# Kernel tuning notes

Measured on AMD Instinct MI355X. Metric: run time of the kernel, lower is better.

The kernel has to match this reference:

```python
import jax, jax.numpy as jnp
import numpy as np

N_NODES = 100000
N_EDGES = 1600000
F_IN, F_HID, F_OUT = 32, 32, 16


def gcn_conv(x, W, b, src, dst):
    """GCNConv: out = D^{-1/2} (A+I) D^{-1/2} X W + b (self-loops already in src/dst)."""
    n = x.shape[0]
    h = x @ W  # [N, F_out]
    deg = jax.ops.segment_sum(jnp.ones(dst.shape[0], x.dtype), dst, num_segments=n)
    dinv = jnp.where(deg > 0, jax.lax.rsqrt(deg), jnp.zeros((), x.dtype))
    coef = dinv[src] * dinv[dst]  # [E_total]
    out = jax.ops.segment_sum(h[src] * coef[:, None], dst, num_segments=n)
    return out + b


def setup_inputs() -> dict:
    key = jax.random.key(0)
    k1, k2, k3, k4, k5, k6, k7 = jax.random.split(key, 7)
    x = jax.random.normal(k1, (N_NODES, F_IN), dtype=jnp.float32)
    edge_index = jax.random.randint(k2, (2, N_EDGES), 0, N_NODES, dtype=jnp.int64)
    s1 = 1.0 / np.sqrt(F_IN)
    s2 = 1.0 / np.sqrt(F_HID)
    W1 = jax.random.uniform(k3, (F_IN, F_HID), jnp.float32, -s1, s1)
    b1 = jax.random.uniform(k4, (F_HID,), jnp.float32, -s1, s1)
    W2 = jax.random.uniform(k5, (F_HID, F_OUT), jnp.float32, -s2, s2)
    b2 = jax.random.uniform(k6, (F_OUT,), jnp.float32, -s2, s2)
    return {"x": x, "edge_index": edge_index, "W1": W1, "b1": b1, "W2": W2, "b2": b2}


def reference(x, edge_index, W1, b1, W2, b2):
    n = x.shape[0]
    loops = jnp.arange(n, dtype=edge_index.dtype)  # GCNConv adds self-loops
    src = jnp.concatenate([edge_index[0], loops])
    dst = jnp.concatenate([edge_index[1], loops])
    h = jnp.tanh(gcn_conv(x, W1, b1, src, dst))
    h = gcn_conv(h, W2, b2, src, dst)
    return h, jax.nn.log_softmax(h, axis=1)
```

## Files before the change

### kernel.cpp

```cpp
#include <hip/hip_runtime.h>
#include <hip/hip_bf16.h>
#include <hip/hip_fp16.h>
#include <math.h>
#include <stdint.h>

#define F_IN  32
#define F_HID 32
#define F_OUT 16
#define NPB     256
#define LOG_NPB 8
#define MAXNB   512
#define BH      256

__device__ inline uint32_t pk_add(uint32_t a, uint32_t b) {
    union { uint32_t u; __half2 h; } x, y, r;
    x.u = a; y.u = b;
    r.h = __hadd2(x.h, y.h);
    return r.u;
}
__device__ inline uint4 pk_add4(uint4 a, uint4 b) {
    a.x = pk_add(a.x, b.x); a.y = pk_add(a.y, b.y);
    a.z = pk_add(a.z, b.z); a.w = pk_add(a.w, b.w);
    return a;
}
__device__ inline uint2 pk_add2(uint2 a, uint2 b) {
    a.x = pk_add(a.x, b.x); a.y = pk_add(a.y, b.y);
    return a;
}

__device__ inline float fexp(float x) {
    return __builtin_amdgcn_exp2f(x * 1.44269504089f);
}
__device__ inline float ftanh(float x) {
    x = fminf(fmaxf(x, -15.f), 15.f);
    float t = __builtin_amdgcn_exp2f(x * 2.88539008178f);
    return (t - 1.0f) * __builtin_amdgcn_rcpf(t + 1.0f);
}

__launch_bounds__(1024)
__global__ void k_hist(const int* __restrict__ ei, int ne, int chunk, int nb,
                       int* __restrict__ hist_mat) {
    __shared__ int hist[MAXNB];
    int t = threadIdx.x, b = blockIdx.x;
    for (int i = t; i < nb; i += 1024) hist[i] = 0;
    __syncthreads();
    long s = (long)b * chunk;
    long e = s + chunk; if (e > ne) e = ne;
    const int* dstp = ei + ne;
    long i = s + (long)t * 4;
    for (; i + 4 <= e; i += 4096) {
        int4 d = *(const int4*)(dstp + i);
        atomicAdd(&hist[d.x >> LOG_NPB], 1);
        atomicAdd(&hist[d.y >> LOG_NPB], 1);
        atomicAdd(&hist[d.z >> LOG_NPB], 1);
        atomicAdd(&hist[d.w >> LOG_NPB], 1);
    }
    if (i < e)
        for (long j = i; j < e; ++j) atomicAdd(&hist[dstp[j] >> LOG_NPB], 1);
    __syncthreads();
    for (int k = t; k < nb; k += 1024)
        hist_mat[(size_t)b * nb + k] = hist[k];
}

__global__ void k_colscan(const int* __restrict__ hist_mat, int* __restrict__ off_mat,
                          int* __restrict__ totalG, int nb) {
    int k = blockIdx.x * 256 + threadIdx.x;
    if (k >= nb) return;
    int run = 0;
    #pragma unroll 8
    for (int b = 0; b < BH; ++b) {
        size_t idx = (size_t)b * nb + k;
        int h = hist_mat[idx];
        off_mat[idx] = run;
        run += h;
    }
    totalG[k] = run;
}

__global__ void k_scanb(const int* __restrict__ totalG, int* __restrict__ boff, int nb) {
    __shared__ int sh[256];
    int t = threadIdx.x;
    int base = t * 2;
    int v[2], s = 0;
    #pragma unroll
    for (int j = 0; j < 2; ++j) {
        v[j] = (base + j < nb) ? totalG[base + j] : 0;
        s += v[j];
    }
    sh[t] = s; __syncthreads();
    for (int o = 1; o < 256; o <<= 1) {
        int u = (t >= o) ? sh[t - o] : 0;
        __syncthreads();
        sh[t] += u;
        __syncthreads();
    }
    int run = sh[t] - s;
    #pragma unroll
    for (int j = 0; j < 2; ++j) {
        int k = base + j;
        if (k < nb) { boff[k] = run; run += v[j]; }
    }
    if (t == 255) boff[nb] = sh[255];
}

__launch_bounds__(1024)
__global__ void k_fillc(const int* __restrict__ ei, int ne, int chunk, int nb,
                        const int* __restrict__ off_mat, const int* __restrict__ boff,
                        uint32_t* __restrict__ ebuf) {
    __shared__ int cur[MAXNB];
    int t = threadIdx.x, b = blockIdx.x;
    for (int i = t; i < nb; i += 1024)
        cur[i] = off_mat[(size_t)b * nb + i] + boff[i];
    __syncthreads();
    long s = (long)b * chunk;
    long e = s + chunk; if (e > ne) e = ne;
    const int* srcp = ei;
    const int* dstp = ei + ne;
    long i = s + (long)t * 4;
    for (; i + 4 <= e; i += 4096) {
        int4 sv = *(const int4*)(srcp + i);
        int4 dv = *(const int4*)(dstp + i);
        int p0 = atomicAdd(&cur[dv.x >> LOG_NPB], 1);
        ebuf[p0] = (uint32_t)sv.x | ((uint32_t)(dv.x & (NPB - 1)) << 17);
        int p1 = atomicAdd(&cur[dv.y >> LOG_NPB], 1);
        ebuf[p1] = (uint32_t)sv.y | ((uint32_t)(dv.y & (NPB - 1)) << 17);
        int p2 = atomicAdd(&cur[dv.z >> LOG_NPB], 1);
        ebuf[p2] = (uint32_t)sv.z | ((uint32_t)(dv.z & (NPB - 1)) << 17);
        int p3 = atomicAdd(&cur[dv.w >> LOG_NPB], 1);
        ebuf[p3] = (uint32_t)sv.w | ((uint32_t)(dv.w & (NPB - 1)) << 17);
    }
    if (i < e) {
        for (long j = i; j < e; ++j) {
            int sn = srcp[j], dn = dstp[j];
            int p = atomicAdd(&cur[dn >> LOG_NPB], 1);
            ebuf[p] = (uint32_t)sn | ((uint32_t)(dn & (NPB - 1)) << 17);
        }
    }
}

__launch_bounds__(256)
__global__ void k_pass2(const uint32_t* __restrict__ ebuf, const int* __restrict__ boff,
                        const float* __restrict__ x,
                        int* __restrict__ csr, int* __restrict__ off_g,
                        float* __restrict__ dinv, uint32_t* __restrict__ xd,
                        int n, int nb) {
    __shared__ int hist[NPB], scn[NPB], cur[NPB];
    __shared__ float sdi[NPB];
    int b = blockIdx.x, t = threadIdx.x;
    int base = boff[b], end = boff[b + 1];
    int v0 = b << LOG_NPB;
    hist[t] = 0;
    __syncthreads();
    for (int i = base + t; i < end; i += 256)
        atomicAdd(&hist[(ebuf[i] >> 17) & (NPB - 1)], 1);
    __syncthreads();
    int val = hist[t];
    scn[t] = val; __syncthreads();
    for (int o = 1; o < 256; o <<= 1) {
        int u = (t >= o) ? scn[t - o] : 0;
        __syncthreads();
        scn[t] += u;
        __syncthreads();
    }
    int excl = scn[t] - val + base;
    cur[t] = excl;
    int v = v0 + t;
    float d = 0.f;
    if (v < n) {
        off_g[v] = excl;
        d = rsqrtf((float)(val + 1));
        dinv[v] = d;
    }
    sdi[t] = d;
    if (b == nb - 1 && t == 0) off_g[n] = end;
    if (b == nb - 1 && t < 16) xd[(size_t)n * 16 + t] = 0u;
    __syncthreads();
    for (int i = base + t; i < end; i += 256) {
        uint32_t r = ebuf[i];
        int slot = atomicAdd(&cur[(r >> 17) & (NPB - 1)], 1);
        csr[slot] = (int)(r & 0x1FFFF);
    }
    for (int i = t; i < NPB * 16; i += 256) {
        int nl = i >> 4, wp = i & 15;
        int vv = v0 + nl;
        if (vv < n) {
            float2 xx = *(const float2*)(x + (size_t)vv * F_IN + 2 * wp);
            float di = sdi[nl];
            union { __half2 h; uint32_t u; } pk;
            pk.h = __floats2half2_rn(xx.x * di, xx.y * di);
            xd[(size_t)vv * 16 + wp] = pk.u;
        }
    }
}

__launch_bounds__(256)
__global__ void k_agg1(const uint32_t* __restrict__ xd, const int* __restrict__ csr,
                       const int* __restrict__ off_g,
                       const float* __restrict__ dinv, const float* __restrict__ b1,
                       const float* __restrict__ W1, const float* __restrict__ W2,
                       uint32_t* __restrict__ g2, int n) {
    __shared__ float W1s[F_IN * F_HID];
    __shared__ float W2s[F_HID * F_OUT];
    __shared__ float sums[8][F_IN + 1];
    __shared__ float hb[8][F_HID + 1];
    int t = threadIdx.x, wv = t >> 6, lane = t & 63;
    ((float4*)W1s)[t] = ((const float4*)W1)[t];
    if (t < 128) ((float4*)W2s)[t] = ((const float4*)W2)[t];
    if (blockIdx.x == 0 && t < 8) g2[(size_t)n * 8 + t] = 0u;
    int half = lane >> 5, l = lane & 31;
    int v = blockIdx.x * 8 + wv * 2 + half;
    bool act = v < n;
    int q = l & 3, slot = l >> 2;
    uint4 acc = make_uint4(0u, 0u, 0u, 0u);
    if (act) {
        if (slot == 0) acc = *(const uint4*)(xd + (size_t)v * 16 + q * 4);
        int start = off_g[v], cnt = off_g[v + 1] - start;
        const int* cp = csr + start;
        int i0 = (slot      < cnt) ? cp[slot]      : n;
        int i1 = (slot + 8  < cnt) ? cp[slot + 8]  : n;
        int i2 = (slot + 16 < cnt) ? cp[slot + 16] : n;
        int i3 = (slot + 24 < cnt) ? cp[slot + 24] : n;
        uint4 w0 = *(const uint4*)(xd + (size_t)i0 * 16 + q * 4);
        uint4 w1 = *(const uint4*)(xd + (size_t)i1 * 16 + q * 4);
        uint4 w2 = *(const uint4*)(xd + (size_t)i2 * 16 + q * 4);
        uint4 w3 = *(const uint4*)(xd + (size_t)i3 * 16 + q * 4);
        acc = pk_add4(acc, w0);
        acc = pk_add4(acc, w1);
        acc = pk_add4(acc, w2);
        acc = pk_add4(acc, w3);
        for (int k = slot + 32; k < cnt; k += 8) {
            int s = cp[k];
            acc = pk_add4(acc, *(const uint4*)(xd + (size_t)s * 16 + q * 4));
        }
    }
    #pragma unroll
    for (int off = 4; off < 32; off <<= 1) {
        acc.x = pk_add(acc.x, (uint32_t)__shfl_xor((int)acc.x, off));
        acc.y = pk_add(acc.y, (uint32_t)__shfl_xor((int)acc.y, off));
        acc.z = pk_add(acc.z, (uint32_t)__shfl_xor((int)acc.z, off));
        acc.w = pk_add(acc.w, (uint32_t)__shfl_xor((int)acc.w, off));
    }
    int ch = l;
    int src = (lane & 32) + (ch >> 3);
    uint32_t a0 = (uint32_t)__shfl((int)acc.x, src);
    uint32_t a1 = (uint32_t)__shfl((int)acc.y, src);
    uint32_t a2 = (uint32_t)__shfl((int)acc.z, src);
    uint32_t a3 = (uint32_t)__shfl((int)acc.w, src);
    int widx = (ch & 7) >> 1;
    uint32_t w = (widx & 2) ? ((widx & 1) ? a3 : a2) : ((widx & 1) ? a1 : a0);
    union { uint32_t u; __half2 h; } pw; pw.u = w;
    float2 f2 = __half22float2(pw.h);
    sums[wv * 2 + half][ch] = (ch & 1) ? f2.y : f2.x;
    __syncthreads();
    {
        int nl = t >> 5, c = t & 31;
        int v1 = blockIdx.x * 8 + nl;
        float di = (v1 < n) ? dinv[v1] : 0.f;
        float s = 0.f;
        #pragma unroll
        for (int k = 0; k < F_IN; ++k) s += sums[nl][k] * W1s[k * F_HID + c];
        hb[nl][c] = ftanh(s * di + b1[c]);
    }
    __syncthreads();
    if (t < 128) {
        int nl = t >> 4, c = t & 15;
        int v2 = blockIdx.x * 8 + nl;
        float s = 0.f;
        #pragma unroll
        for (int k = 0; k < F_HID; ++k) s += hb[nl][k] * W2s[k * F_OUT + c];
        float gv = (v2 < n) ? s * dinv[v2] : 0.f;
        float hi2 = __shfl_xor(gv, 1);
        if ((c & 1) == 0 && v2 < n) {
            union { __half2 h; uint32_t u; } pk2;
            pk2.h = __floats2half2_rn(gv, hi2);
            g2[(size_t)v2 * 8 + (c >> 1)] = pk2.u;
        }
    }
}

__launch_bounds__(256)
__global__ void k_agg2(const uint32_t* __restrict__ g2, const int* __restrict__ csr,
                       const int* __restrict__ off_g,
                       const float* __restrict__ dinv, const float* __restrict__ b2,
                       float* __restrict__ out_h, float* __restrict__ out_ls, int n) {
    int t = threadIdx.x, wv = t >> 6, lane = t & 63;
    int half = lane >> 5, l = lane & 31;
    int v = blockIdx.x * 8 + wv * 2 + half;
    bool act = v < n;
    int q = l & 3, slot = l >> 2;
    uint2 acc = make_uint2(0u, 0u);
    if (act) {
        if (slot == 0) acc = *(const uint2*)(g2 + (size_t)v * 8 + q * 2);
        int start = off_g[v], cnt = off_g[v + 1] - start;
        const int* cp = csr + start;
        int i0 = (slot      < cnt) ? cp[slot]      : n;
        int i1 = (slot + 8  < cnt) ? cp[slot + 8]  : n;
        int i2 = (slot + 16 < cnt) ? cp[slot + 16] : n;
        int i3 = (slot + 24 < cnt) ? cp[slot + 24] : n;
        uint2 w0 = *(const uint2*)(g2 + (size_t)i0 * 8 + q * 2);
        uint2 w1 = *(const uint2*)(g2 + (size_t)i1 * 8 + q * 2);
        uint2 w2 = *(const uint2*)(g2 + (size_t)i2 * 8 + q * 2);
        uint2 w3 = *(const uint2*)(g2 + (size_t)i3 * 8 + q * 2);
        acc = pk_add2(acc, w0);
        acc = pk_add2(acc, w1);
        acc = pk_add2(acc, w2);
        acc = pk_add2(acc, w3);
        for (int k = slot + 32; k < cnt; k += 8) {
            int s = cp[k];
            acc = pk_add2(acc, *(const uint2*)(g2 + (size_t)s * 8 + q * 2));
        }
    }
    #pragma unroll
    for (int off = 4; off < 32; off <<= 1) {
        acc.x = pk_add(acc.x, (uint32_t)__shfl_xor((int)acc.x, off));
        acc.y = pk_add(acc.y, (uint32_t)__shfl_xor((int)acc.y, off));
    }
    if (l < 16) {
        int ch = l;
        int src = (lane & 32) + (ch >> 2);
        uint32_t a0 = (uint32_t)__shfl((int)acc.x, src);
        uint32_t a1 = (uint32_t)__shfl((int)acc.y, src);
        uint32_t w = (ch & 2) ? a1 : a0;
        union { uint32_t u; __half2 h; } pw; pw.u = w;
        float2 f2 = __half22float2(pw.h);
        float f = (ch & 1) ? f2.y : f2.x;
        float di = act ? dinv[v] : 0.f;
        float val = f * di + b2[ch];
        float m = val;
        m = fmaxf(m, __shfl_xor(m, 1));
        m = fmaxf(m, __shfl_xor(m, 2));
        m = fmaxf(m, __shfl_xor(m, 4));
        m = fmaxf(m, __shfl_xor(m, 8));
        float S = fexp(val - m);
        S += __shfl_xor(S, 1);
        S += __shfl_xor(S, 2);
        S += __shfl_xor(S, 4);
        S += __shfl_xor(S, 8);
        float L = __builtin_amdgcn_logf(S) * 0.69314718056f + m;
        if (act) {
            out_h[(size_t)v * F_OUT + ch]  = val;
            out_ls[(size_t)v * F_OUT + ch] = val - L;
        }
    }
}

static inline size_t align16(size_t x) { return (x + 15) & ~(size_t)15; }

extern "C" void kernel_launch(void* const* d_in, const int* in_sizes, int n_in,
                              void* d_out, int out_size, void* d_ws, size_t ws_size,
                              hipStream_t stream) {
    const float* x  = (const float*)d_in[0];
    const int*   ei = (const int*)d_in[1];
    const float* W1 = (const float*)d_in[2];
    const float* b1 = (const float*)d_in[3];
    const float* W2 = (const float*)d_in[4];
    const float* b2 = (const float*)d_in[5];

    int n  = in_sizes[0] / F_IN;
    int ne = in_sizes[1] / 2;
    int nb = (n + NPB - 1) / NPB;
    int chunk = (((ne + BH - 1) / BH) + 3) & ~3;

    float* out_h  = (float*)d_out;
    float* out_ls = out_h + (size_t)n * F_OUT;

    char* p = (char*)d_ws;
    float*    dinv     = (float*)p;    p += align16((size_t)n * sizeof(float));
    int*      totalG   = (int*)p;      p += align16(MAXNB * sizeof(int));
    int*      boff     = (int*)p;      p += align16((MAXNB + 4) * sizeof(int));
    int*      off_g    = (int*)p;      p += align16(((size_t)n + 4) * sizeof(int));
    int*      hist_mat = (int*)p;      p += align16((size_t)BH * nb * sizeof(int));
    int*      off_mat  = (int*)p;      p += align16((size_t)BH * nb * sizeof(int));
    uint32_t* ebuf     = (uint32_t*)p; p += align16((size_t)ne * sizeof(uint32_t));
    int*      csr      = (int*)p;      p += align16((size_t)ne * sizeof(int));
    uint32_t* xd       = (uint32_t*)p; p += align16(((size_t)n + 1) * 16 * sizeof(uint32_t));
    uint32_t* g2       = (uint32_t*)p; p += align16(((size_t)n + 1) * 8 * sizeof(uint32_t));

    k_hist   <<<BH, 1024, 0, stream>>>(ei, ne, chunk, nb, hist_mat);
    k_colscan<<<(nb + 255) / 256, 256, 0, stream>>>(hist_mat, off_mat, totalG, nb);
    k_scanb  <<<1, 256, 0, stream>>>(totalG, boff, nb);
    k_fillc  <<<BH, 1024, 0, stream>>>(ei, ne, chunk, nb, off_mat, boff, ebuf);
    k_pass2  <<<nb, 256, 0, stream>>>(ebuf, boff, x, csr, off_g, dinv, xd, n, nb);

    k_agg1   <<<(n + 7) / 8, 256, 0, stream>>>(xd, csr, off_g, dinv, b1, W1, W2, g2, n);
    k_agg2   <<<(n + 7) / 8, 256, 0, stream>>>(g2, csr, off_g, dinv, b2, out_h, out_ls, n);
}
```

Measured before the change: 109.5 us.

## Widen histogram grid, replicate shared histograms, and wave-parallelize column scan

New measurement: 101.5 us. 1.08x faster.

```diff
diff --git a/kernel.cpp b/kernel.cpp
--- a/kernel.cpp
+++ b/kernel.cpp
@@ -10,7 +10,7 @@
 #define NPB     256
 #define LOG_NPB 8
 #define MAXNB   512
-#define BH      256
+#define BH      512
 
 __device__ inline uint32_t pk_add(uint32_t a, uint32_t b) {
     union { uint32_t u; __half2 h; } x, y, r;
@@ -37,44 +37,53 @@
     return (t - 1.0f) * __builtin_amdgcn_rcpf(t + 1.0f);
 }
 
-__launch_bounds__(1024)
+__launch_bounds__(512)
 __global__ void k_hist(const int* __restrict__ ei, int ne, int chunk, int nb,
                        int* __restrict__ hist_mat) {
-    __shared__ int hist[MAXNB];
+    __shared__ int hist[4][MAXNB];
     int t = threadIdx.x, b = blockIdx.x;
-    for (int i = t; i < nb; i += 1024) hist[i] = 0;
+    int rep = t >> 7;
+    for (int i = t; i < 4 * MAXNB; i += 512) ((int*)hist)[i] = 0;
     __syncthreads();
     long s = (long)b * chunk;
     long e = s + chunk; if (e > ne) e = ne;
     const int* dstp = ei + ne;
     long i = s + (long)t * 4;
-    for (; i + 4 <= e; i += 4096) {
+    for (; i + 4 <= e; i += 2048) {
         int4 d = *(const int4*)(dstp + i);
-        atomicAdd(&hist[d.x >> LOG_NPB], 1);
-        atomicAdd(&hist[d.y >> LOG_NPB], 1);
-        atomicAdd(&hist[d.z >> LOG_NPB], 1);
-        atomicAdd(&hist[d.w >> LOG_NPB], 1);
+        atomicAdd(&hist[rep][d.x >> LOG_NPB], 1);
+        atomicAdd(&hist[rep][d.y >> LOG_NPB], 1);
+        atomicAdd(&hist[rep][d.z >> LOG_NPB], 1);
+        atomicAdd(&hist[rep][d.w >> LOG_NPB], 1);
     }
     if (i < e)
-        for (long j = i; j < e; ++j) atomicAdd(&hist[dstp[j] >> LOG_NPB], 1);
-    __syncthreads();
-    for (int k = t; k < nb; k += 1024)
-        hist_mat[(size_t)b * nb + k] = hist[k];
-}
-
+        for (long j = i; j < e; ++j) atomicAdd(&hist[rep][dstp[j] >> LOG_NPB], 1);
+    __syncthreads();
+    for (int k = t; k < nb; k += 512)
+        hist_mat[(size_t)b * nb + k] = hist[0][k] + hist[1][k] + hist[2][k] + hist[3][k];
+}
+
+__launch_bounds__(64)
 __global__ void k_colscan(const int* __restrict__ hist_mat, int* __restrict__ off_mat,
                           int* __restrict__ totalG, int nb) {
-    int k = blockIdx.x * 256 + threadIdx.x;
+    int k = blockIdx.x;
     if (k >= nb) return;
+    int lane = threadIdx.x;
     int run = 0;
-    #pragma unroll 8
-    for (int b = 0; b < BH; ++b) {
-        size_t idx = (size_t)b * nb + k;
-        int h = hist_mat[idx];
-        off_mat[idx] = run;
-        run += h;
-    }
-    totalG[k] = run;
+    #pragma unroll
+    for (int c = 0; c < BH; c += 64) {
+        size_t idx = (size_t)(c + lane) * nb + k;
+        int v = hist_mat[idx];
+        int inc = v;
+        #pragma unroll
+        for (int o = 1; o < 64; o <<= 1) {
+            int u = __shfl_up(inc, o);
+            if (lane >= o) inc += u;
+        }
+        off_mat[idx] = run + inc - v;
+        run += __shfl(inc, 63);
+    }
+    if (lane == 0) totalG[k] = run;
 }
 
 __global__ void k_scanb(const int* __restrict__ totalG, int* __restrict__ boff, int nb) {
@@ -103,13 +112,13 @@
     if (t == 255) boff[nb] = sh[255];
 }
 
-__launch_bounds__(1024)
+__launch_bounds__(512)
 __global__ void k_fillc(const int* __restrict__ ei, int ne, int chunk, int nb,
                         const int* __restrict__ off_mat, const int* __restrict__ boff,
                         uint32_t* __restrict__ ebuf) {
     __shared__ int cur[MAXNB];
     int t = threadIdx.x, b = blockIdx.x;
-    for (int i = t; i < nb; i += 1024)
+    for (int i = t; i < nb; i += 512)
         cur[i] = off_mat[(size_t)b * nb + i] + boff[i];
     __syncthreads();
     long s = (long)b * chunk;
@@ -117,7 +126,7 @@
     const int* srcp = ei;
     const int* dstp = ei + ne;
     long i = s + (long)t * 4;
-    for (; i + 4 <= e; i += 4096) {
+    for (; i + 4 <= e; i += 2048) {
         int4 sv = *(const int4*)(srcp + i);
         int4 dv = *(const int4*)(dstp + i);
         int p0 = atomicAdd(&cur[dv.x >> LOG_NPB], 1);
@@ -376,10 +385,10 @@
     uint32_t* xd       = (uint32_t*)p; p += align16(((size_t)n + 1) * 16 * sizeof(uint32_t));
     uint32_t* g2       = (uint32_t*)p; p += align16(((size_t)n + 1) * 8 * sizeof(uint32_t));
 
-    k_hist   <<<BH, 1024, 0, stream>>>(ei, ne, chunk, nb, hist_mat);
-    k_colscan<<<(nb + 255) / 256, 256, 0, stream>>>(hist_mat, off_mat, totalG, nb);
+    k_hist   <<<BH, 512, 0, stream>>>(ei, ne, chunk, nb, hist_mat);
+    k_colscan<<<nb, 64, 0, stream>>>(hist_mat, off_mat, totalG, nb);
     k_scanb  <<<1, 256, 0, stream>>>(totalG, boff, nb);
-    k_fillc  <<<BH, 1024, 0, stream>>>(ei, ne, chunk, nb, off_mat, boff, ebuf);
+    k_fillc  <<<BH, 512, 0, stream>>>(ei, ne, chunk, nb, off_mat, boff, ebuf);
     k_pass2  <<<nb, 256, 0, stream>>>(ebuf, boff, x, csr, off_g, dinv, xd, n, nb);
 
     k_agg1   <<<(n + 7) / 8, 256, 0, stream>>>(xd, csr, off_g, dinv, b1, W1, W2, g2, n);
```
